# Optimization experiments

Measured on AMD Instinct MI355X. Metric: run time of the kernel, lower is better.

Reference implementation:

```python
import jax, jax.numpy as jnp
import numpy as np

B, T, D = 2, 1024, 1024
H, KV, HD = 16, 4, 64
L, VP = 6, 32000
SOFTCAP = 15.0
WINDOWS = [256, 1024, 256, 1024, 256, 1024]  # 'SL' pattern, last layer forced long
VE_LAYERS = {1: 0, 3: 1, 5: 2}               # layer_idx -> index into stacked ve params
GATE_CH = 12   # min(12, n_embd)
SMEAR_CH = 24  # min(24, n_embd)


def _rms(x):
    # F.rms_norm with default eps = finfo(dtype).eps
    return x / jnp.sqrt(jnp.mean(x * x, axis=-1, keepdims=True) + jnp.finfo(x.dtype).eps)


def _rope(x, cos, sin):
    x1, x2 = x[..., :HD // 2], x[..., HD // 2:]
    return jnp.concatenate([x1 * cos + x2 * sin, -x1 * sin + x2 * cos], axis=-1)


def _rotary_tables():
    inv = 1.0 / (100000.0 ** (np.arange(0, HD, 2, dtype=np.float32) / HD))
    f = np.arange(T, dtype=np.float32)[:, None] * inv[None, :]
    return jnp.asarray(np.cos(f))[None, :, None, :], jnp.asarray(np.sin(f))[None, :, None, :]


def setup_inputs() -> dict:
    key = jax.random.key(0)
    ks = jax.random.split(key, 12)
    scale = (3.0 ** 0.5) * D ** -0.5
    u = lambda k, s, a: jax.random.uniform(k, s, jnp.float32, -a, a)
    return {
        "input_ids": jax.random.randint(ks[0], (B, T), 0, VP),
        "wte": 0.8 * jax.random.normal(ks[1], (VP, D), jnp.float32),
        "Wq": u(ks[2], (L, H * HD, D), scale),
        "Wk": u(ks[3], (L, KV * HD, D), scale),
        "Wv": u(ks[4], (L, KV * HD, D), scale),
        "Wo": 0.02 * jax.random.normal(ks[5], (L, D, D), jnp.float32),
        "Wfc": u(ks[6], (L, 4 * D, D), 0.4 * scale),
        "Wmp": 0.02 * jax.random.normal(ks[7], (L, D, 4 * D), jnp.float32),
        "ve_tab": u(ks[8], (len(VE_LAYERS), VP, KV * HD), scale),
        "ve_gate_w": jax.random.uniform(ks[9], (len(VE_LAYERS), KV, GATE_CH), jnp.float32, 0.0, 0.02),
        "lm_w": 0.001 * jax.random.normal(ks[10], (VP, D), jnp.float32),
        "resid_l": jnp.asarray([1.15 - 0.1 * i / (L - 1) for i in range(L)], jnp.float32),
        "x0_l": jnp.asarray([0.2 - 0.15 * i / (L - 1) for i in range(L)], jnp.float32),
        "smear_w": u(ks[11], (1, SMEAR_CH), scale),
        "smear_l": 0.1 * jnp.ones((1,), jnp.float32),
    }


def _attention(x, ids, Wq, Wk, Wv, Wo, ve_tab, ve_gate_w, cos, sin, mask):
    q = jnp.einsum('btd,ed->bte', x, Wq).reshape(B, T, H, HD)
    k = jnp.einsum('btd,ed->bte', x, Wk).reshape(B, T, KV, HD)
    v = jnp.einsum('btd,ed->bte', x, Wv).reshape(B, T, KV, HD)
    if ve_tab is not None:
        ve = ve_tab[ids].reshape(B, T, KV, HD)
        gate = 3.0 * jax.nn.sigmoid(jnp.einsum('btc,kc->btk', x[..., :GATE_CH], ve_gate_w))
        v = v + gate[..., None] * ve
    q = _rms(_rope(q, cos, sin)) * 1.2
    k = _rms(_rope(k, cos, sin)) * 1.2
    rep = H // KV
    k = jnp.repeat(k, rep, axis=2)  # matches expand+reshape head-major layout
    v = jnp.repeat(v, rep, axis=2)
    scores = jnp.einsum('bqhd,bkhd->bhqk', q, k) / (HD ** 0.5)
    scores = jnp.where(mask, scores, jnp.finfo(scores.dtype).min)
    att = jax.nn.softmax(scores, axis=-1)
    y = jnp.einsum('bhqk,bkhd->bqhd', att, v).reshape(B, T, H * HD)
    return jnp.einsum('btd,ed->bte', y, Wo)


def _forward(input_ids, wte, Wq, Wk, Wv, Wo, Wfc, Wmp, ve_tab, ve_gate_w,
             lm_w, resid_l, x0_l, smear_w, smear_l):
    cos, sin = _rotary_tables()
    x = _rms(wte[input_ids])
    # smear: mix each token embedding with the previous token, gated
    gate = smear_l * jax.nn.sigmoid(jnp.einsum('btc,oc->bto', x[:, 1:, :SMEAR_CH], smear_w))
    x = jnp.concatenate([x[:, :1], x[:, 1:] + gate * x[:, :-1]], axis=1)
    x0 = x
    i = jnp.arange(T)
    diff = i[:, None] - i[None, :]
    for l in range(L):
        mask = ((diff >= 0) & (diff < WINDOWS[l]))[None, None]  # [1,1,T,T]
        x = resid_l[l] * x + x0_l[l] * x0
        vi = VE_LAYERS.get(l)
        h = _attention(_rms(x), input_ids, Wq[l], Wk[l], Wv[l], Wo[l],
                       ve_tab[vi] if vi is not None else None,
                       ve_gate_w[vi] if vi is not None else None,
                       cos, sin, mask)
        x = x + h
        hidden = jnp.square(jax.nn.relu(jnp.einsum('btd,fd->btf', _rms(x), Wfc[l])))
        x = x + jnp.einsum('btf,of->bto', hidden, Wmp[l])
    x = _rms(x)
    logits = jnp.einsum('btd,vd->btv', x, lm_w)
    return SOFTCAP * jnp.tanh(logits / SOFTCAP)


def reference(input_ids, wte, Wq, Wk, Wv, Wo, Wfc, Wmp, ve_tab, ve_gate_w,
              lm_w, resid_l, x0_l, smear_w, smear_l):
    return _forward(input_ids, wte, Wq, Wk, Wv, Wo, Wfc, Wmp, ve_tab, ve_gate_w,
                    lm_w, resid_l, x0_l, smear_w, smear_l)
```

## Files before the change

### kernel.cpp

```cpp
#include <hip/hip_runtime.h>
#include <stdint.h>
#include <math.h>


using bf16x8 = __attribute__((ext_vector_type(8))) short;
using f32x4  = __attribute__((ext_vector_type(4))) float;

#define DEV static __device__ __forceinline__

DEV unsigned short f2bf(float f) {
  unsigned int x = __builtin_bit_cast(unsigned int, f);
  x += 0x7fffu + ((x >> 16) & 1u);
  return (unsigned short)(x >> 16);
}
DEV float bf2f(unsigned short u) {
  return __builtin_bit_cast(float, (unsigned int)u << 16);
}
DEV unsigned int packbf2(float a, float b) {
  return (unsigned int)f2bf(a) | ((unsigned int)f2bf(b) << 16);
}

DEV void gload16(const unsigned short* g, unsigned short* l) {
  __builtin_amdgcn_global_load_lds(
      (__attribute__((address_space(1))) void*)const_cast<unsigned short*>(g),
      (__attribute__((address_space(3))) void*)l, 16, 0, 0);
}


extern "C" __global__ __launch_bounds__(256)
void prep_weights_kernel(const float* __restrict__ Wq, const float* __restrict__ Wk,
                         const float* __restrict__ Wv, const float* __restrict__ Wo,
                         const float* __restrict__ Wfc, const float* __restrict__ Wmp,
                         const float* __restrict__ LmW,
                         unsigned short* __restrict__ wqkv, unsigned short* __restrict__ wo,
                         unsigned short* __restrict__ wfc, unsigned short* __restrict__ wmp,
                         unsigned short* __restrict__ wlm) {
  const long v = (long)blockIdx.x * 256 + threadIdx.x;
  const long S0 = 1179648, S1 = S0 + 786432, S2 = S1 + 3145728,
             S3 = S2 + 3145728, S4 = S3 + 4096000;
  const float* src; unsigned short* dst;
  if (v < S0) {
    const long i = v * 8;
    const int c = (int)(i & 1023);
    const int row = (int)(i >> 10);
    const int l = row / 1536, r = row - l * 1536;
    if (r < 1024)      src = Wq + ((size_t)l * 1024 + r) * 1024 + c;
    else if (r < 1280) src = Wk + ((size_t)l * 256 + (r - 1024)) * 1024 + c;
    else               src = Wv + ((size_t)l * 256 + (r - 1280)) * 1024 + c;
    dst = wqkv + i;
  } else if (v < S1) {
    const long i = (v - S0) * 8; src = Wo + i;  dst = wo + i;
  } else if (v < S2) {
    const long i = (v - S1) * 8; src = Wfc + i; dst = wfc + i;
  } else if (v < S3) {
    const long i = (v - S2) * 8; src = Wmp + i; dst = wmp + i;
  } else if (v < S4) {
    const long i = (v - S3) * 8; src = LmW + i; dst = wlm + i;
  } else {
    return;
  }
  const float4 a = *reinterpret_cast<const float4*>(src);
  const float4 b = *reinterpret_cast<const float4*>(src + 4);
  uint4 u;
  u.x = packbf2(a.x, a.y); u.y = packbf2(a.z, a.w);
  u.z = packbf2(b.x, b.y); u.w = packbf2(b.z, b.w);
  *reinterpret_cast<uint4*>(dst) = u;
}


extern "C" __global__ __launch_bounds__(256)
void rope_tab_kernel(float* __restrict__ cost, float* __restrict__ sint) {
  const int idx = blockIdx.x * 256 + threadIdx.x;
  const int t = idx >> 5, i = idx & 31;
  const double inv = exp(((double)i * (-1.0 / 32.0)) * log(100000.0));
  const double f = (double)t * inv;
  cost[idx] = (float)cos(f);
  sint[idx] = (float)sin(f);
}


extern "C" __global__ __launch_bounds__(256)
void embed_kernel(const int* __restrict__ ids, const float* __restrict__ wte,
                  const float* __restrict__ smear_w, const float* __restrict__ smear_l,
                  const float* __restrict__ residc, const float* __restrict__ x0c,
                  float* __restrict__ x, float* __restrict__ x0,
                  unsigned short* __restrict__ xn) {
  const int wid = threadIdx.x >> 6, lane = threadIdx.x & 63;
  const int tok = blockIdx.x * 4 + wid;
  const int t = tok & 1023;
  const float eps = 1.1920929e-7f;

  const float* wrow = wte + (size_t)ids[tok] * 1024;
  float4 v[4];
  float ss = 0.f;
#pragma unroll
  for (int i = 0; i < 4; ++i) {
    v[i] = *reinterpret_cast<const float4*>(wrow + i * 256 + lane * 4);
    ss += v[i].x * v[i].x + v[i].y * v[i].y + v[i].z * v[i].z + v[i].w * v[i].w;
  }
#pragma unroll
  for (int m = 1; m < 64; m <<= 1) ss += __shfl_xor(ss, m);
  const float sc = 1.f / sqrtf(ss * (1.f / 1024.f) + eps);

  float4 pv[4];
#pragma unroll
  for (int i = 0; i < 4; ++i) { pv[i].x = 0.f; pv[i].y = 0.f; pv[i].z = 0.f; pv[i].w = 0.f; }
  float scp = 0.f, gate = 0.f;
  if (t > 0) {
    const float* prow = wte + (size_t)ids[tok - 1] * 1024;
    float ssp = 0.f;
#pragma unroll
    for (int i = 0; i < 4; ++i) {
      pv[i] = *reinterpret_cast<const float4*>(prow + i * 256 + lane * 4);
      ssp += pv[i].x * pv[i].x + pv[i].y * pv[i].y + pv[i].z * pv[i].z + pv[i].w * pv[i].w;
    }
#pragma unroll
    for (int m = 1; m < 64; m <<= 1) ssp += __shfl_xor(ssp, m);
    scp = 1.f / sqrtf(ssp * (1.f / 1024.f) + eps);
    float gp = 0.f;
    if (lane < 6) {
      gp = v[0].x * smear_w[lane * 4] + v[0].y * smear_w[lane * 4 + 1] +
           v[0].z * smear_w[lane * 4 + 2] + v[0].w * smear_w[lane * 4 + 3];
      gp *= sc;
    }
#pragma unroll
    for (int m = 1; m < 64; m <<= 1) gp += __shfl_xor(gp, m);
    gate = smear_l[0] / (1.f + __expf(-gp));
  }
  const float a0 = residc[0], b0 = x0c[0];
  float4 y[4];
  float ssy = 0.f;
#pragma unroll
  for (int i = 0; i < 4; ++i) {
    const int c = i * 256 + lane * 4;
    float4 o;
    o.x = v[i].x * sc + gate * pv[i].x * scp;
    o.y = v[i].y * sc + gate * pv[i].y * scp;
    o.z = v[i].z * sc + gate * pv[i].z * scp;
    o.w = v[i].w * sc + gate * pv[i].w * scp;
    *reinterpret_cast<float4*>(x0 + (size_t)tok * 1024 + c) = o;
    float4 yy;
    yy.x = a0 * o.x + b0 * o.x; yy.y = a0 * o.y + b0 * o.y;
    yy.z = a0 * o.z + b0 * o.z; yy.w = a0 * o.w + b0 * o.w;
    *reinterpret_cast<float4*>(x + (size_t)tok * 1024 + c) = yy;
    y[i] = yy;
    ssy += yy.x * yy.x + yy.y * yy.y + yy.z * yy.z + yy.w * yy.w;
  }
#pragma unroll
  for (int m = 1; m < 64; m <<= 1) ssy += __shfl_xor(ssy, m);
  const float scy = 1.f / sqrtf(ssy * (1.f / 1024.f) + eps);
#pragma unroll
  for (int i = 0; i < 4; ++i) {
    const int c = i * 256 + lane * 4;
    ushort4 u;
    u.x = f2bf(y[i].x * scy); u.y = f2bf(y[i].y * scy);
    u.z = f2bf(y[i].z * scy); u.w = f2bf(y[i].w * scy);
    *reinterpret_cast<ushort4*>(xn + (size_t)tok * 1024 + c) = u;
  }
}


extern "C" __global__ __launch_bounds__(256)
void rmsnorm_kernel(float* __restrict__ x, const float* __restrict__ x0,
                    const float* __restrict__ parts, int np,
                    const float* __restrict__ residc, const float* __restrict__ x0c,
                    int layer, int combine, unsigned short* __restrict__ xn) {
  const int wid = threadIdx.x >> 6, lane = threadIdx.x & 63;
  const int tok = blockIdx.x * 4 + wid;
  float* xr = x + (size_t)tok * 1024;
  const float* x0r = x0 + (size_t)tok * 1024;
  float a = 1.f, bb = 0.f;
  if (combine) { a = residc[layer]; bb = x0c[layer]; }
  float4 v[4];
  float ss = 0.f;
#pragma unroll
  for (int i = 0; i < 4; ++i) {
    const int c = i * 256 + lane * 4;
    float4 xv = *reinterpret_cast<const float4*>(xr + c);
    for (int pi = 0; pi < np; ++pi) {
      const float4 pv = *reinterpret_cast<const float4*>(
          parts + (size_t)pi * 2048 * 1024 + (size_t)tok * 1024 + c);
      xv.x += pv.x; xv.y += pv.y; xv.z += pv.z; xv.w += pv.w;
    }
    if (combine) {
      const float4 ov = *reinterpret_cast<const float4*>(x0r + c);
      xv.x = a * xv.x + bb * ov.x; xv.y = a * xv.y + bb * ov.y;
      xv.z = a * xv.z + bb * ov.z; xv.w = a * xv.w + bb * ov.w;
    }
    if (combine || np > 0) *reinterpret_cast<float4*>(xr + c) = xv;
    v[i] = xv;
    ss += xv.x * xv.x + xv.y * xv.y + xv.z * xv.z + xv.w * xv.w;
  }
#pragma unroll
  for (int m = 1; m < 64; m <<= 1) ss += __shfl_xor(ss, m);
  const float sc = 1.f / sqrtf(ss * (1.f / 1024.f) + 1.1920929e-7f);
#pragma unroll
  for (int i = 0; i < 4; ++i) {
    const int c = i * 256 + lane * 4;
    ushort4 u;
    u.x = f2bf(v[i].x * sc); u.y = f2bf(v[i].y * sc);
    u.z = f2bf(v[i].z * sc); u.w = f2bf(v[i].w * sc);
    *reinterpret_cast<ushort4*>(xn + (size_t)tok * 1024 + c) = u;
  }
}


extern "C" __global__ __launch_bounds__(256)
void qkv_post_kernel(const float* __restrict__ qkv0, const float* __restrict__ qkv1,
                     const unsigned short* __restrict__ xn,
                     const int* __restrict__ ids,
                     const float* __restrict__ ve_tab, const float* __restrict__ ve_gate_w,
                     const float* __restrict__ cost, const float* __restrict__ sint,
                     unsigned short* __restrict__ qb, unsigned short* __restrict__ kbuf,
                     unsigned short* __restrict__ vb) {
  const int wid = threadIdx.x >> 6, lane = threadIdx.x & 63;
  const int tok = blockIdx.x * 4 + wid;
  const int t = tok & 1023;
  const float eps = 1.1920929e-7f;
  const float* rowA = qkv0 + (size_t)tok * 1536;
  const float* rowB = qkv1 + (size_t)tok * 1536;
  const bool x1half = (lane & 2) == 0;
  const int i0 = (lane & 1) << 4;

  {
    float v[16], p[16];
    {
      const float4* ra = reinterpret_cast<const float4*>(rowA + lane * 16);
      const float4* rb = reinterpret_cast<const float4*>(rowB + lane * 16);
#pragma unroll
      for (int i = 0; i < 4; ++i) {
        const float4 qa = ra[i], qb4 = rb[i];
        v[i * 4] = qa.x + qb4.x; v[i * 4 + 1] = qa.y + qb4.y;
        v[i * 4 + 2] = qa.z + qb4.z; v[i * 4 + 3] = qa.w + qb4.w;
      }
    }
#pragma unroll
    for (int i = 0; i < 16; ++i) p[i] = __shfl_xor(v[i], 2);
    float out[16]; float ssq = 0.f;
#pragma unroll
    for (int i = 0; i < 16; ++i) {
      const float c = cost[t * 32 + i0 + i];
      const float s = sint[t * 32 + i0 + i];
      out[i] = x1half ? (v[i] * c + p[i] * s) : (v[i] * c - p[i] * s);
      ssq += out[i] * out[i];
    }
    ssq += __shfl_xor(ssq, 1);
    ssq += __shfl_xor(ssq, 2);
    const float sc = 0.15f / sqrtf(ssq * (1.f / 64.f) + eps);
#pragma unroll
    for (int i = 0; i < 16; i += 4) {
      ushort4 u;
      u.x = f2bf(out[i] * sc); u.y = f2bf(out[i + 1] * sc);
      u.z = f2bf(out[i + 2] * sc); u.w = f2bf(out[i + 3] * sc);
      *reinterpret_cast<ushort4*>(qb + (size_t)tok * 1024 + lane * 16 + i) = u;
    }
  }
  const int kl = lane & 15;
  {
    float v[16], p[16];
    {
      const float4* ra = reinterpret_cast<const float4*>(rowA + 1024 + kl * 16);
      const float4* rb = reinterpret_cast<const float4*>(rowB + 1024 + kl * 16);
#pragma unroll
      for (int i = 0; i < 4; ++i) {
        const float4 qa = ra[i], qb4 = rb[i];
        v[i * 4] = qa.x + qb4.x; v[i * 4 + 1] = qa.y + qb4.y;
        v[i * 4 + 2] = qa.z + qb4.z; v[i * 4 + 3] = qa.w + qb4.w;
      }
    }
#pragma unroll
    for (int i = 0; i < 16; ++i) p[i] = __shfl_xor(v[i], 2);
    float out[16]; float ssq = 0.f;
#pragma unroll
    for (int i = 0; i < 16; ++i) {
      const float c = cost[t * 32 + i0 + i];
      const float s = sint[t * 32 + i0 + i];
      out[i] = x1half ? (v[i] * c + p[i] * s) : (v[i] * c - p[i] * s);
      ssq += out[i] * out[i];
    }
    ssq += __shfl_xor(ssq, 1);
    ssq += __shfl_xor(ssq, 2);
    const float sc = 1.2f / sqrtf(ssq * (1.f / 64.f) + eps);
    if (lane < 16) {
#pragma unroll
      for (int i = 0; i < 16; i += 4) {
        ushort4 u;
        u.x = f2bf(out[i] * sc); u.y = f2bf(out[i + 1] * sc);
        u.z = f2bf(out[i + 2] * sc); u.w = f2bf(out[i + 3] * sc);
        *reinterpret_cast<ushort4*>(kbuf + (size_t)tok * 256 + kl * 16 + i) = u;
      }
    }
  }
  {
    float v[16];
    {
      const float4* ra = reinterpret_cast<const float4*>(rowA + 1280 + kl * 16);
      const float4* rb = reinterpret_cast<const float4*>(rowB + 1280 + kl * 16);
#pragma unroll
      for (int i = 0; i < 4; ++i) {
        const float4 qa = ra[i], qb4 = rb[i];
        v[i * 4] = qa.x + qb4.x; v[i * 4 + 1] = qa.y + qb4.y;
        v[i * 4 + 2] = qa.z + qb4.z; v[i * 4 + 3] = qa.w + qb4.w;
      }
    }
    if (ve_tab != nullptr) {
      const int kvh = kl >> 2;
      float g = 0.f;
#pragma unroll
      for (int c = 0; c < 12; ++c)
        g += bf2f(xn[(size_t)tok * 1024 + c]) * ve_gate_w[kvh * 12 + c];
      g = 3.f / (1.f + __expf(-g));
      const float* ver = ve_tab + (size_t)ids[tok] * 256 + kl * 16;
#pragma unroll
      for (int i = 0; i < 16; ++i) v[i] += g * ver[i];
    }
    if (lane < 16) {
#pragma unroll
      for (int i = 0; i < 16; i += 4) {
        ushort4 u;
        u.x = f2bf(v[i]); u.y = f2bf(v[i + 1]); u.z = f2bf(v[i + 2]); u.w = f2bf(v[i + 3]);
        *reinterpret_cast<ushort4*>(vb + (size_t)tok * 256 + kl * 16 + i) = u;
      }
    }
  }
}


extern "C" __global__ __launch_bounds__(256)
void vtrans_kernel(const unsigned short* __restrict__ vb, unsigned short* __restrict__ vt) {
  __shared__ unsigned short tile[64][72];
  const int t0 = blockIdx.x << 6;
  const int bk = blockIdx.y;
  const int tid = threadIdx.x;
  {
    const int r = tid >> 2, cs = (tid & 3) << 4;
    const unsigned short* src = vb + ((size_t)((bk >> 2) * 1024 + t0 + r)) * 256 + (bk & 3) * 64 + cs;
    *reinterpret_cast<uint4*>(&tile[r][cs]) = *reinterpret_cast<const uint4*>(src);
    *reinterpret_cast<uint4*>(&tile[r][cs + 8]) = *reinterpret_cast<const uint4*>(src + 8);
  }
  __syncthreads();
  {
    const int d = tid >> 2, ts = (tid & 3) << 4;
    unsigned int w[8];
#pragma unroll
    for (int i = 0; i < 8; ++i)
      w[i] = (unsigned int)tile[ts + 2 * i][d] | ((unsigned int)tile[ts + 2 * i + 1][d] << 16);
    unsigned short* dst = vt + ((size_t)bk * 64 + d) * 1024 + t0 + ts;
    uint4 u0; u0.x = w[0]; u0.y = w[1]; u0.z = w[2]; u0.w = w[3];
    uint4 u1; u1.x = w[4]; u1.y = w[5]; u1.z = w[6]; u1.w = w[7];
    *reinterpret_cast<uint4*>(dst) = u0;
    *reinterpret_cast<uint4*>(dst + 8) = u1;
  }
}


extern "C" __global__ __launch_bounds__(64)
void attn_kernel(const unsigned short* __restrict__ qb,
                 const unsigned short* __restrict__ kb,
                 const unsigned short* __restrict__ vt,
                 unsigned short* __restrict__ y, int W) {
  __shared__ unsigned short p_lds[16 * 32];
  const int lane = threadIdx.x;
  const int q0 = blockIdx.x << 4;
  const int h = blockIdx.y;
  const int b = blockIdx.z;
  const int kv = h >> 2;
  const int lr = lane & 15, lk = lane >> 4;

  bf16x8 qf0, qf1;
  {
    const unsigned short* qrow = qb + ((size_t)(b * 1024 + q0 + lr)) * 1024 + h * 64 + (lk << 3);
    qf0 = *reinterpret_cast<const bf16x8*>(qrow);
    qf1 = *reinterpret_cast<const bf16x8*>(qrow + 32);
  }
  f32x4 acc[4] = {};
  float m_run = -3e38f, l_run = 0.f;
  int kstart = q0 - W + 1; if (kstart < 0) kstart = 0;
  kstart &= ~31;
  const int qq = q0 + lr;

  for (int kb0 = kstart; kb0 < q0 + 16; kb0 += 32) {
    f32x4 st[2];
#pragma unroll
    for (int s = 0; s < 2; ++s) {
      const unsigned short* krow = kb + ((size_t)(b * 1024 + kb0 + (s << 4) + lr)) * 256 + kv * 64 + (lk << 3);
      bf16x8 kf0 = *reinterpret_cast<const bf16x8*>(krow);
      bf16x8 kf1 = *reinterpret_cast<const bf16x8*>(krow + 32);
      f32x4 z = {0.f, 0.f, 0.f, 0.f};
      z = __builtin_amdgcn_mfma_f32_16x16x32_bf16(kf0, qf0, z, 0, 0, 0);
      st[s] = __builtin_amdgcn_mfma_f32_16x16x32_bf16(kf1, qf1, z, 0, 0, 0);
    }
    float sv[8];
    float bm = -3e38f;
#pragma unroll
    for (int s = 0; s < 2; ++s)
#pragma unroll
      for (int j = 0; j < 4; ++j) {
        const int key = kb0 + (s << 4) + (lk << 2) + j;
        const bool valid = (key <= qq) && (qq - key < W);
        const float xx = valid ? st[s][j] : -3e38f;
        sv[s * 4 + j] = xx;
        bm = fmaxf(bm, xx);
      }
    bm = fmaxf(bm, __shfl_xor(bm, 16));
    bm = fmaxf(bm, __shfl_xor(bm, 32));
    const float m_new = fmaxf(m_run, bm);
    const float alpha = __expf(m_run - m_new);
    float psum = 0.f;
    unsigned short pbv[8];
#pragma unroll
    for (int s = 0; s < 2; ++s)
#pragma unroll
      for (int j = 0; j < 4; ++j) {
        const int key = kb0 + (s << 4) + (lk << 2) + j;
        const bool valid = (key <= qq) && (qq - key < W);
        const float pv = valid ? __expf(sv[s * 4 + j] - m_new) : 0.f;
        psum += pv;
        pbv[s * 4 + j] = f2bf(pv);
      }
    psum += __shfl_xor(psum, 16);
    psum += __shfl_xor(psum, 32);
    l_run = l_run * alpha + psum;
    m_run = m_new;

    __syncthreads();
    {
      ushort4 u0, u1;
      u0.x = pbv[0]; u0.y = pbv[1]; u0.z = pbv[2]; u0.w = pbv[3];
      u1.x = pbv[4]; u1.y = pbv[5]; u1.z = pbv[6]; u1.w = pbv[7];
      *reinterpret_cast<ushort4*>(p_lds + lr * 32 + (lk << 2)) = u0;
      *reinterpret_cast<ushort4*>(p_lds + lr * 32 + 16 + (lk << 2)) = u1;
    }
    __syncthreads();
    const bf16x8 pf = *reinterpret_cast<const bf16x8*>(p_lds + lr * 32 + (lk << 3));
    float al[4];
#pragma unroll
    for (int j = 0; j < 4; ++j) al[j] = __shfl(alpha, (lk << 2) + j);
#pragma unroll
    for (int d = 0; d < 4; ++d) {
      const unsigned short* vrow = vt + ((size_t)((b * 4 + kv) * 64 + (d << 4) + lr)) * 1024 + kb0 + (lk << 3);
      const bf16x8 vf = *reinterpret_cast<const bf16x8*>(vrow);
#pragma unroll
      for (int j = 0; j < 4; ++j) acc[d][j] *= al[j];
      acc[d] = __builtin_amdgcn_mfma_f32_16x16x32_bf16(pf, vf, acc[d], 0, 0, 0);
    }
  }
  float linv[4];
#pragma unroll
  for (int j = 0; j < 4; ++j) linv[j] = 1.f / __shfl(l_run, (lk << 2) + j);
#pragma unroll
  for (int d = 0; d < 4; ++d)
#pragma unroll
    for (int j = 0; j < 4; ++j) {
      const int qrow = q0 + (lk << 2) + j;
      y[((size_t)(b * 1024 + qrow)) * 1024 + h * 64 + (d << 4) + lr] = f2bf(acc[d][j] * linv[j]);
    }
}


template <int EPI>
__global__ __launch_bounds__(512)
void gemm512(const unsigned short* __restrict__ A,
             const unsigned short* __restrict__ Bw,
             void* __restrict__ Cout,
             int M, int N, int K, int kchunk) {
  __shared__ unsigned short sA[2][128 * 32];
  __shared__ unsigned short sB[2][128 * 32];
  const int tid = threadIdx.x;

  int flat = blockIdx.x + gridDim.x * blockIdx.y;
  const int nwg = gridDim.x * gridDim.y;
  if ((nwg & 7) == 0) flat = (flat & 7) * (nwg >> 3) + (flat >> 3);
  const int m0 = (flat % gridDim.x) << 7;
  const int n0 = (flat / gridDim.x) << 7;
  const int k_begin = blockIdx.z * kchunk;
  int k_end = k_begin + kchunk; if (k_end > K) k_end = K;

  const int wid = tid >> 6, lane = tid & 63;
  const int wr = wid >> 2, wc = wid & 3;
  const int lr = lane & 15, lk = lane >> 4;

  const int row0 = tid >> 2;
  const int srcch = (((tid & 3) - (tid >> 3)) & 3) << 3;
  const unsigned short* gA = A + (size_t)(m0 + row0) * K + srcch;
  const unsigned short* gB = Bw + (size_t)(n0 + row0) * K + srcch;

  auto stage = [&](int buf, int k0) {
    gload16(gA + k0, sA[buf] + tid * 8);
    gload16(gB + k0, sB[buf] + tid * 8);
  };

  int aoff[4], boff[2];
#pragma unroll
  for (int i = 0; i < 4; ++i) {
    const int r = (wr << 6) + (i << 4) + lr;
    aoff[i] = r * 32 + (((lk + (r >> 1)) & 3) << 3);
  }
#pragma unroll
  for (int j = 0; j < 2; ++j) {
    const int r = (wc << 5) + (j << 4) + lr;
    boff[j] = r * 32 + (((lk + (r >> 1)) & 3) << 3);
  }

  f32x4 acc[4][2] = {};
  int cur = 0;
  stage(0, k_begin);
  __syncthreads();
  for (int k0 = k_begin; k0 < k_end; k0 += 32) {
    bf16x8 af[4], bfr[2];
#pragma unroll
    for (int i = 0; i < 4; ++i)
      af[i] = *reinterpret_cast<const bf16x8*>(sA[cur] + aoff[i]);
#pragma unroll
    for (int j = 0; j < 2; ++j)
      bfr[j] = *reinterpret_cast<const bf16x8*>(sB[cur] + boff[j]);
    const int nxt = k0 + 32;
    if (nxt < k_end) stage(cur ^ 1, nxt);
#pragma unroll
    for (int i = 0; i < 4; ++i)
#pragma unroll
      for (int j = 0; j < 2; ++j)
        acc[i][j] = __builtin_amdgcn_mfma_f32_16x16x32_bf16(bfr[j], af[i], acc[i][j], 0, 0, 0);
    __syncthreads();
    cur ^= 1;
  }
  const int mbase = m0 + (wr << 6) + lr;
  const int nbase = n0 + (wc << 5) + (lk << 2);
  float* outF = (float*)Cout + (size_t)blockIdx.z * M * N;
#pragma unroll
  for (int i = 0; i < 4; ++i)
#pragma unroll
    for (int j = 0; j < 2; ++j) {
      const int m = mbase + (i << 4);
      const int n = nbase + (j << 4);
      const size_t off = (size_t)m * N + n;
      f32x4 v = acc[i][j];
      if (EPI == 0) {
        *reinterpret_cast<f32x4*>(outF + off) = v;
      } else if (EPI == 2) {
        ushort4 u;
        float r0 = v[0] > 0.f ? v[0] : 0.f;
        float r1 = v[1] > 0.f ? v[1] : 0.f;
        float r2 = v[2] > 0.f ? v[2] : 0.f;
        float r3 = v[3] > 0.f ? v[3] : 0.f;
        u.x = f2bf(r0 * r0); u.y = f2bf(r1 * r1);
        u.z = f2bf(r2 * r2); u.w = f2bf(r3 * r3);
        *reinterpret_cast<ushort4*>((unsigned short*)Cout + off) = u;
      } else {
        f32x4 o;
#pragma unroll
        for (int e = 0; e < 4; ++e) {
          const float ex = __expf(v[e] * (2.f / 15.f));
          o[e] = 15.f - 30.f / (ex + 1.f);
        }
        *reinterpret_cast<f32x4*>((float*)Cout + off) = o;
      }
    }
}


template <int EPI, int NJ>
__global__ __launch_bounds__(256)
void gemm_bf16(const unsigned short* __restrict__ A,
               const unsigned short* __restrict__ Bw,
               const float* __restrict__ Cin, void* __restrict__ Cout,
               int M, int N, int K, int kchunk) {
  constexpr int BN = NJ * 32;
  __shared__ unsigned short sA[2][128 * 32];
  __shared__ unsigned short sB[2][BN * 32];
  const int tid = threadIdx.x;

  int flat = blockIdx.x + gridDim.x * blockIdx.y;
  const int nwg = gridDim.x * gridDim.y;
  if ((nwg & 7) == 0) flat = (flat & 7) * (nwg >> 3) + (flat >> 3);
  const int m0 = (flat % gridDim.x) << 7;
  const int n0 = (flat / gridDim.x) * BN;
  const int k_begin = blockIdx.z * kchunk;
  int k_end = k_begin + kchunk; if (k_end > K) k_end = K;

  const int wid = tid >> 6, lane = tid & 63;
  const int wr = wid >> 1, wc = wid & 1;
  const int lr = lane & 15, lk = lane >> 4;

  const int row0 = tid >> 2, ch0 = (tid & 3) << 3;
  const unsigned short* gA0 = A + (size_t)(m0 + row0) * K + ch0;
  const unsigned short* gA1 = gA0 + (size_t)64 * K;
  const unsigned short* gB0 = Bw + (size_t)(n0 + row0) * K + ch0;
  const int lofs = wid << 9;

  auto stage = [&](int buf, int k0) {
    gload16(gA0 + k0, sA[buf] + lofs);
    gload16(gA1 + k0, sA[buf] + lofs + 2048);
    gload16(gB0 + k0, sB[buf] + lofs);
  };

  f32x4 acc[4][NJ] = {};
  int cur = 0;
  stage(0, k_begin);
  __syncthreads();
  for (int k0 = k_begin; k0 < k_end; k0 += 32) {
    bf16x8 af[4], bfr[NJ];
#pragma unroll
    for (int i = 0; i < 4; ++i)
      af[i] = *reinterpret_cast<const bf16x8*>(sA[cur] + ((wr << 6) + (i << 4) + lr) * 32 + (lk << 3));
#pragma unroll
    for (int j = 0; j < NJ; ++j)
      bfr[j] = *reinterpret_cast<const bf16x8*>(sB[cur] + (wc * (BN / 2) + (j << 4) + lr) * 32 + (lk << 3));
    const int nxt = k0 + 32;
    if (nxt < k_end) stage(cur ^ 1, nxt);
#pragma unroll
    for (int i = 0; i < 4; ++i)
#pragma unroll
      for (int j = 0; j < NJ; ++j)
        acc[i][j] = __builtin_amdgcn_mfma_f32_16x16x32_bf16(bfr[j], af[i], acc[i][j], 0, 0, 0);
    __syncthreads();
    cur ^= 1;
  }
  const int mbase = m0 + (wr << 6) + lr;
  const int nbase = n0 + wc * (BN / 2) + (lk << 2);
  float* outF = (float*)Cout + (size_t)blockIdx.z * M * N;
#pragma unroll
  for (int i = 0; i < 4; ++i)
#pragma unroll
    for (int j = 0; j < NJ; ++j) {
      const int m = mbase + (i << 4);
      const int n = nbase + (j << 4);
      const size_t off = (size_t)m * N + n;
      *reinterpret_cast<f32x4*>(outF + off) = acc[i][j];
    }
  (void)Cin;
}


extern "C" void kernel_launch(void* const* d_in, const int* in_sizes, int n_in,
                              void* d_out, int out_size, void* d_ws, size_t ws_size,
                              hipStream_t stream) {
  (void)in_sizes; (void)n_in; (void)out_size; (void)ws_size;
  const int*   ids  = (const int*)  d_in[0];
  const float* wte  = (const float*)d_in[1];
  const float* Wq   = (const float*)d_in[2];
  const float* Wk   = (const float*)d_in[3];
  const float* Wv   = (const float*)d_in[4];
  const float* Wo   = (const float*)d_in[5];
  const float* Wfc  = (const float*)d_in[6];
  const float* Wmp  = (const float*)d_in[7];
  const float* VeT  = (const float*)d_in[8];
  const float* VeG  = (const float*)d_in[9];
  const float* LmW  = (const float*)d_in[10];
  const float* ResC = (const float*)d_in[11];
  const float* X0C  = (const float*)d_in[12];
  const float* SmW  = (const float*)d_in[13];
  const float* SmL  = (const float*)d_in[14];

  char* p = (char*)d_ws;
  auto alloc = [&](size_t bytes) -> char* {
    char* r = p; p += (bytes + 255) & ~(size_t)255; return r;
  };
  float* x  = (float*)alloc((size_t)2048 * 1024 * 4);
  float* x0 = (float*)alloc((size_t)2048 * 1024 * 4);
  unsigned short* xn = (unsigned short*)alloc((size_t)2048 * 1024 * 2);
  unsigned short* hidden = (unsigned short*)alloc((size_t)2048 * 4096 * 2);
  float* qkvp = (float*)alloc((size_t)2 * 2048 * 1536 * 4);
  float* wop  = (float*)alloc((size_t)2 * 2048 * 1024 * 4);
  float* mpp  = (float*)alloc((size_t)4 * 2048 * 1024 * 4);
  unsigned short* qbuf = (unsigned short*)alloc((size_t)2048 * 1024 * 2);
  unsigned short* kbuf = (unsigned short*)alloc((size_t)2048 * 256 * 2);
  unsigned short* vbuf = (unsigned short*)alloc((size_t)2048 * 256 * 2);
  unsigned short* vtb  = (unsigned short*)alloc((size_t)2048 * 256 * 2);
  unsigned short* ybuf = (unsigned short*)alloc((size_t)2048 * 1024 * 2);
  float* cost = (float*)alloc((size_t)1024 * 32 * 4);
  float* sint = (float*)alloc((size_t)1024 * 32 * 4);
  unsigned short* wqkv = (unsigned short*)alloc((size_t)6 * 1536 * 1024 * 2);
  unsigned short* wo   = (unsigned short*)alloc((size_t)6 * 1024 * 1024 * 2);
  unsigned short* wfc  = (unsigned short*)alloc((size_t)6 * 4096 * 1024 * 2);
  unsigned short* wmp  = (unsigned short*)alloc((size_t)6 * 1024 * 4096 * 2);
  unsigned short* wlm  = (unsigned short*)alloc((size_t)32000 * 1024 * 2);

  prep_weights_kernel<<<48256, 256, 0, stream>>>(Wq, Wk, Wv, Wo, Wfc, Wmp, LmW,
                                                 wqkv, wo, wfc, wmp, wlm);
  rope_tab_kernel<<<128, 256, 0, stream>>>(cost, sint);
  embed_kernel<<<512, 256, 0, stream>>>(ids, wte, SmW, SmL, ResC, X0C, x, x0, xn);

  static const int WIN[6] = {256, 1024, 256, 1024, 256, 1024};
  for (int l = 0; l < 6; ++l) {
    if (l > 0)
      rmsnorm_kernel<<<512, 256, 0, stream>>>(x, x0, mpp, 4, ResC, X0C, l, 1, xn);
    gemm512<0><<<dim3(16, 12, 2), 512, 0, stream>>>(xn, wqkv + (size_t)l * 1536 * 1024,
                                                    qkvp, 2048, 1536, 1024, 512);
    const float* vtab = nullptr; const float* vgw = nullptr;
    if (l == 1 || l == 3 || l == 5) {
      const int vi = (l - 1) / 2;
      vtab = VeT + (size_t)vi * 32000 * 256;
      vgw  = VeG + vi * 48;
    }
    qkv_post_kernel<<<512, 256, 0, stream>>>(qkvp, qkvp + (size_t)2048 * 1536, xn, ids,
                                             vtab, vgw, cost, sint, qbuf, kbuf, vbuf);
    vtrans_kernel<<<dim3(16, 8), 256, 0, stream>>>(vbuf, vtb);
    attn_kernel<<<dim3(64, 16, 2), 64, 0, stream>>>(qbuf, kbuf, vtb, ybuf, WIN[l]);
    gemm_bf16<0, 2><<<dim3(16, 16, 2), 256, 0, stream>>>(ybuf, wo + (size_t)l * 1024 * 1024,
                                                         nullptr, wop, 2048, 1024, 1024, 512);
    rmsnorm_kernel<<<512, 256, 0, stream>>>(x, x0, wop, 2, ResC, X0C, l, 0, xn);
    gemm512<2><<<dim3(16, 32), 512, 0, stream>>>(xn, wfc + (size_t)l * 4096 * 1024,
                                                 hidden, 2048, 4096, 1024, 1024);
    gemm512<0><<<dim3(16, 8, 4), 512, 0, stream>>>(hidden, wmp + (size_t)l * 1024 * 4096,
                                                   mpp, 2048, 1024, 4096, 1024);
  }
  rmsnorm_kernel<<<512, 256, 0, stream>>>(x, x0, mpp, 4, ResC, X0C, 0, 0, xn);
  gemm512<3><<<dim3(16, 250), 512, 0, stream>>>(xn, wlm, (float*)d_out,
                                                2048, 32000, 1024, 1024);
}
```

Measured before the change: 1.379 ms.

## Use 256x256-tile GEMM kernel for final LM-head projection with softcap

```diff
diff --git a/kernel.cpp b/kernel.cpp
--- a/kernel.cpp
+++ b/kernel.cpp
@@ -460,6 +460,132 @@
 
 template <int EPI>
 __global__ __launch_bounds__(512)
+void gemm256(const unsigned short* __restrict__ A,
+             const unsigned short* __restrict__ Bw,
+             void* __restrict__ Cout, int M, int N, int K) {
+  __shared__ unsigned short sA[2][16384];
+  __shared__ unsigned short sB[2][16384];
+  const int tid = threadIdx.x;
+
+  int flat = blockIdx.x + gridDim.x * blockIdx.y;
+  const int nwg = gridDim.x * gridDim.y;
+  if ((nwg & 7) == 0) flat = (flat & 7) * (nwg >> 3) + (flat >> 3);
+  const int m0 = (flat % gridDim.x) << 8;
+  const int n0 = (flat / gridDim.x) << 8;
+
+  const int wid = tid >> 6, lane = tid & 63;
+  const int wr = wid >> 2, wc = wid & 3;
+  const int lr = lane & 15, lk = lane >> 4;
+
+  const int srow = tid >> 2, scol = (tid & 3) << 3;
+  const unsigned short* gA = A + (size_t)(m0 + srow) * K + scol;
+  const unsigned short* gB = Bw + (size_t)(n0 + srow) * K + scol;
+  const size_t rstep = (size_t)128 * K;
+
+  const int NT = K >> 6;
+
+  auto stageA = [&](int buf, int tau, int kk) {
+    const int kc = (tau << 6) + (kk << 5);
+    unsigned short* d = sA[buf] + kk * 8192 + tid * 8;
+    gload16(gA + kc, d);
+    gload16(gA + rstep + kc, d + 4096);
+  };
+  auto stageB = [&](int buf, int tau, int kk) {
+    const int kc = (tau << 6) + (kk << 5);
+    unsigned short* d = sB[buf] + kk * 8192 + tid * 8;
+    gload16(gB + kc, d);
+    gload16(gB + rstep + kc, d + 4096);
+  };
+
+  stageA(0, 0, 0); stageB(0, 0, 0);
+  stageA(0, 0, 1); stageB(0, 0, 1);
+  stageA(1, 1, 0); stageB(1, 1, 0);
+
+  f32x4 acc[8][4] = {};
+  for (int t = 0; t < NT; ++t) {
+    const int cb = t & 1;
+    {
+      int tn = t + 1; if (tn >= NT) tn = NT - 1;
+      stageA(cb ^ 1, tn, 1);
+      stageB(cb ^ 1, tn, 1);
+    }
+    asm volatile("s_waitcnt vmcnt(8)" ::: "memory");
+    __builtin_amdgcn_s_barrier();
+    __builtin_amdgcn_sched_barrier(0);
+    {
+      bf16x8 af[8], bfr[4];
+#pragma unroll
+      for (int i = 0; i < 8; ++i)
+        af[i] = *reinterpret_cast<const bf16x8*>(
+            sA[cb] + ((wr << 7) + (i << 4) + lr) * 32 + (lk << 3));
+#pragma unroll
+      for (int j = 0; j < 4; ++j)
+        bfr[j] = *reinterpret_cast<const bf16x8*>(
+            sB[cb] + ((wc << 6) + (j << 4) + lr) * 32 + (lk << 3));
+#pragma unroll
+      for (int i = 0; i < 8; ++i)
+#pragma unroll
+        for (int j = 0; j < 4; ++j)
+          acc[i][j] = __builtin_amdgcn_mfma_f32_16x16x32_bf16(bfr[j], af[i], acc[i][j], 0, 0, 0);
+    }
+    __builtin_amdgcn_s_barrier();
+    __builtin_amdgcn_sched_barrier(0);
+    {
+      int tn = t + 2; if (tn >= NT) tn = NT - 1;
+      stageA(cb, tn, 0);
+      stageB(cb, tn, 0);
+    }
+    asm volatile("s_waitcnt vmcnt(8)" ::: "memory");
+    __builtin_amdgcn_s_barrier();
+    __builtin_amdgcn_sched_barrier(0);
+    {
+      bf16x8 af[8], bfr[4];
+#pragma unroll
+      for (int i = 0; i < 8; ++i)
+        af[i] = *reinterpret_cast<const bf16x8*>(
+            sA[cb] + 8192 + ((wr << 7) + (i << 4) + lr) * 32 + (lk << 3));
+#pragma unroll
+      for (int j = 0; j < 4; ++j)
+        bfr[j] = *reinterpret_cast<const bf16x8*>(
+            sB[cb] + 8192 + ((wc << 6) + (j << 4) + lr) * 32 + (lk << 3));
+#pragma unroll
+      for (int i = 0; i < 8; ++i)
+#pragma unroll
+        for (int j = 0; j < 4; ++j)
+          acc[i][j] = __builtin_amdgcn_mfma_f32_16x16x32_bf16(bfr[j], af[i], acc[i][j], 0, 0, 0);
+    }
+    __builtin_amdgcn_s_barrier();
+    __builtin_amdgcn_sched_barrier(0);
+  }
+  asm volatile("s_waitcnt vmcnt(0)" ::: "memory");
+
+  const int mbase = m0 + (wr << 7) + lr;
+  const int nbase = n0 + (wc << 6) + (lk << 2);
+#pragma unroll
+  for (int i = 0; i < 8; ++i)
+#pragma unroll
+    for (int j = 0; j < 4; ++j) {
+      const int m = mbase + (i << 4);
+      const int n = nbase + (j << 4);
+      const size_t off = (size_t)m * N + n;
+      f32x4 v = acc[i][j];
+      if (EPI == 0) {
+        *reinterpret_cast<f32x4*>((float*)Cout + off) = v;
+      } else {
+        f32x4 o;
+#pragma unroll
+        for (int e = 0; e < 4; ++e) {
+          const float ex = __expf(v[e] * (2.f / 15.f));
+          o[e] = 15.f - 30.f / (ex + 1.f);
+        }
+        *reinterpret_cast<f32x4*>((float*)Cout + off) = o;
+      }
+    }
+}
+
+
+template <int EPI>
+__global__ __launch_bounds__(512)
 void gemm512(const unsigned short* __restrict__ A,
              const unsigned short* __restrict__ Bw,
              void* __restrict__ Cout,
@@ -706,6 +832,6 @@
                                                    mpp, 2048, 1024, 4096, 1024);
   }
   rmsnorm_kernel<<<512, 256, 0, stream>>>(x, x0, mpp, 4, ResC, X0C, 0, 0, xn);
-  gemm512<3><<<dim3(16, 250), 512, 0, stream>>>(xn, wlm, (float*)d_out,
-                                                2048, 32000, 1024, 1024);
-}
+  gemm256<3><<<dim3(8, 125), 512, 0, stream>>>(xn, wlm, (float*)d_out,
+                                               2048, 32000, 1024);
+}
```

Measured after the change: 1.390 ms. No clear change (+0.8%).
